# Kernel optimization log

Measured on AMD Instinct MI355X. Metric: run time of the kernel, lower is better.

The kernel has to match this reference:

```python
import jax, jax.numpy as jnp
import numpy as np

NHEAD, DK, DV, DMODEL, L = 8, 64, 64, 512, 32

def setup_inputs() -> dict:
    key = jax.random.key(0)
    ks = jax.random.split(key, 9)
    B, N = 4, 2048
    s = 1.0 / np.sqrt(DMODEL)
    return {
        "q": jax.random.normal(ks[0], (B, N, DMODEL), jnp.float32),
        "k": jax.random.normal(ks[1], (B, N, DMODEL), jnp.float32),
        "v": jax.random.normal(ks[2], (B, N, DMODEL), jnp.float32),
        "Wq": jax.random.normal(ks[3], (DMODEL, NHEAD * DK), jnp.float32) * s,
        "Wk": jax.random.normal(ks[4], (DMODEL, NHEAD * DK), jnp.float32) * s,
        "Wv": jax.random.normal(ks[5], (DMODEL, NHEAD * DV), jnp.float32) * s,
        "Wfc": jax.random.normal(ks[6], (NHEAD * DV, DMODEL), jnp.float32) * s,
        "ln_g": jnp.ones((DMODEL,), jnp.float32),
        "ln_b": jnp.zeros((DMODEL,), jnp.float32),
    }

def reference(q, k, v, Wq, Wk, Wv, Wfc, ln_g, ln_b):
    B, Nq, _ = q.shape
    residual = q
    # project and split heads: [B, H, N, d]
    qh = (q @ Wq).reshape(B, Nq, NHEAD, DK).transpose(0, 2, 1, 3)
    kh = (k @ Wk).reshape(B, k.shape[1], NHEAD, DK).transpose(0, 2, 1, 3)
    vh = (v @ Wv).reshape(B, v.shape[1], NHEAD, DV).transpose(0, 2, 1, 3)
    # scaled dot-product scores and softmax over keys
    attn = jnp.einsum('bhqd,bhkd->bhqk', qh / jnp.sqrt(jnp.float32(DK)), kh)
    attn = jax.nn.softmax(attn, axis=-1)
    # AWG: keep entries >= l-th largest per row, renormalize
    threshold = jax.lax.top_k(attn, L)[0][..., -1:]  # [B,H,Nq,1]
    W = jnp.where(attn >= threshold, attn, 0.0)
    W_out = W / jnp.sum(W, axis=-1, keepdims=True)
    out = jnp.einsum('bhqk,bhkd->bhqd', W_out, vh)
    out = out.transpose(0, 2, 1, 3).reshape(B, Nq, NHEAD * DV)
    out = out @ Wfc + residual
    # LayerNorm, eps=1e-6
    mu = jnp.mean(out, axis=-1, keepdims=True)
    var = jnp.var(out, axis=-1, keepdims=True)
    return (out - mu) / jnp.sqrt(var + 1e-6) * ln_g + ln_b
```

## Files before the change

### kernel.cpp

```cpp
#include <hip/hip_runtime.h>
#include <hip/hip_fp16.h>

#define BATCH 4
#define NSEQ 2048
#define DMODEL 512
#define NHEAD 8
#define HDIM 64
#define LSEL 32
#define SROWU 2056
#define MAXL 128

typedef __attribute__((ext_vector_type(8))) _Float16 f16x8;
typedef __attribute__((ext_vector_type(4))) float f32x4;

__device__ inline ushort f2h(float x) { __half h = __float2half(x); return *reinterpret_cast<ushort*>(&h); }
__device__ inline uint h2sort(ushort h) { return (h & 0x8000u) ? (uint)(h ^ 0xFFFFu) : (uint)(h | 0x8000u); }
__device__ inline float sort2f(uint su) {
    ushort hb = (su & 0x8000u) ? (ushort)(su ^ 0x8000u) : (ushort)(su ^ 0xFFFFu);
    __half th; *reinterpret_cast<ushort*>(&th) = hb;
    return __half2float(th);
}

__global__ __launch_bounds__(256) void cvtW_kernel(
    const float* __restrict__ Wq, const float* __restrict__ Wk,
    const float* __restrict__ Wv, const float* __restrict__ Wfc,
    ushort* __restrict__ Wt)
{
    const int z = blockIdx.y;
    const float* W = (z == 0) ? Wq : (z == 1) ? Wk : (z == 2) ? Wv : Wfc;
    ushort* O = Wt + (size_t)z * DMODEL * DMODEL;
    const int gt = blockIdx.x * 256 + threadIdx.x;
    const int n = gt & 511;
    const int kc = (gt >> 9) * 16;
    uint pk[8];
#pragma unroll
    for (int i = 0; i < 8; ++i) {
        uint lo = f2h(W[(size_t)(kc + 2 * i) * DMODEL + n]);
        uint hi = f2h(W[(size_t)(kc + 2 * i + 1) * DMODEL + n]);
        pk[i] = lo | (hi << 16);
    }
    uint4 u0 = {pk[0], pk[1], pk[2], pk[3]};
    uint4 u1 = {pk[4], pk[5], pk[6], pk[7]};
    *(uint4*)(O + (size_t)n * DMODEL + kc) = u0;
    *(uint4*)(O + (size_t)n * DMODEL + kc + 8) = u1;
}

template<int MODE>
__global__ __launch_bounds__(256, 2) void hgemm_kernel(
    const float* __restrict__ Fq, const float* __restrict__ Fk, const float* __restrict__ Fv,
    const ushort* __restrict__ A16,
    const ushort* __restrict__ Wt,
    ushort* __restrict__ O0, ushort* __restrict__ O1, ushort* __restrict__ O2,
    float* __restrict__ Ofc)
{
    __shared__ ushort Ah[64][40];
    __shared__ ushort Bh[512][40];

    const int tid = threadIdx.x;
    const int wave = tid >> 6, lane = tid & 63;
    const int lr = lane & 15, lg = lane >> 4;
    const int bm = blockIdx.x * 64;
    const int z = blockIdx.y;

    const float* Af = (MODE == 0) ? (z == 0 ? Fq : z == 1 ? Fk : Fv) : nullptr;
    const ushort* Wz = Wt + (size_t)((MODE == 0) ? z : 3) * (DMODEL * DMODEL);

    f32x4 acc[4][8];
#pragma unroll
    for (int i = 0; i < 4; ++i)
#pragma unroll
        for (int j = 0; j < 8; ++j) acc[i][j] = (f32x4){0.f, 0.f, 0.f, 0.f};

    const int sar = tid >> 2, sak = (tid & 3) * 8;

    for (int k0 = 0; k0 < DMODEL; k0 += 32) {
        __syncthreads();
        if (MODE == 0) {
            float4 fa = *(const float4*)(Af + (size_t)(bm + sar) * DMODEL + k0 + sak);
            float4 fb = *(const float4*)(Af + (size_t)(bm + sar) * DMODEL + k0 + sak + 4);
            uint4 pk;
            pk.x = (uint)f2h(fa.x) | ((uint)f2h(fa.y) << 16);
            pk.y = (uint)f2h(fa.z) | ((uint)f2h(fa.w) << 16);
            pk.z = (uint)f2h(fb.x) | ((uint)f2h(fb.y) << 16);
            pk.w = (uint)f2h(fb.z) | ((uint)f2h(fb.w) << 16);
            *(uint4*)&Ah[sar][sak] = pk;
        } else {
            *(uint4*)&Ah[sar][sak] = *(const uint4*)(A16 + (size_t)(bm + sar) * DMODEL + k0 + sak);
        }
#pragma unroll
        for (int i = 0; i < 8; ++i) {
            int n = sar + 64 * i;
            *(uint4*)&Bh[n][sak] = *(const uint4*)(Wz + (size_t)n * DMODEL + k0 + sak);
        }
        __syncthreads();
        f16x8 af[4];
#pragma unroll
        for (int fr = 0; fr < 4; ++fr) af[fr] = *(const f16x8*)&Ah[fr * 16 + lr][lg * 8];
#pragma unroll
        for (int fc2 = 0; fc2 < 8; ++fc2) {
            f16x8 bf = *(const f16x8*)&Bh[wave * 128 + fc2 * 16 + lr][lg * 8];
#pragma unroll
            for (int fr = 0; fr < 4; ++fr)
                acc[fr][fc2] = __builtin_amdgcn_mfma_f32_16x16x32_f16(af[fr], bf, acc[fr][fc2], 0, 0, 0);
        }
    }

    if (MODE == 1) {
#pragma unroll
        for (int fr = 0; fr < 4; ++fr)
#pragma unroll
            for (int fc2 = 0; fc2 < 8; ++fc2)
#pragma unroll
                for (int r = 0; r < 4; ++r)
                    Ofc[(size_t)(bm + fr * 16 + lg * 4 + r) * DMODEL + wave * 128 + fc2 * 16 + lr] = acc[fr][fc2][r];
        return;
    }

    ushort* O = (z == 0) ? O0 : (z == 1) ? O1 : O2;
    const int b = bm >> 11;
    const int nseq0 = bm & (NSEQ - 1);
    ushort* smw = (ushort*)&Bh[0][0] + wave * (64 * 72);
#pragma unroll
    for (int hp = 0; hp < 2; ++hp) {
        __syncthreads();
#pragma unroll
        for (int f4 = 0; f4 < 4; ++f4) {
            int fc2 = hp * 4 + f4;
            int nl = f4 * 16 + lr;
#pragma unroll
            for (int fr = 0; fr < 4; ++fr)
#pragma unroll
                for (int r = 0; r < 4; ++r)
                    smw[(fr * 16 + lg * 4 + r) * 72 + nl] = f2h(acc[fr][fc2][r]);
        }
        __syncthreads();
        const int h = wave * 2 + hp;
        ushort* obase = O + ((size_t)(b * NHEAD + h) * NSEQ + nseq0) * HDIM;
#pragma unroll
        for (int i = 0; i < 8; ++i) {
            int m = i * 8 + (lane >> 3);
            int dc = (lane & 7) * 8;
            *(uint4*)(obase + (size_t)m * HDIM + dc) = *(const uint4*)(smw + m * 72 + dc);
        }
    }
}

__device__ inline int wave_sum6(int c) {
    int tot = (int)__popcll(__ballot(c & 1));
    tot += (int)__popcll(__ballot(c & 2)) << 1;
    tot += (int)__popcll(__ballot(c & 4)) << 2;
    tot += (int)__popcll(__ballot(c & 8)) << 3;
    tot += (int)__popcll(__ballot(c & 16)) << 4;
    tot += (int)__popcll(__ballot(c & 32)) << 5;
    return tot;
}

__device__ uint full_thr(const ushort* Sr, int lane, uint lo0) {
    uint flo = lo0, fhi = 0xFFFFu;
#pragma unroll 1
    for (int it2 = 0; it2 < 16; ++it2) {
        uint mid = (flo + fhi + 1) >> 1, M = mid << 16;
        int cl = 0;
#pragma unroll
        for (int it = 0; it < 4; ++it) {
            uint4 r4 = *(const uint4*)(Sr + it * 512 + lane * 8);
            cl += ((r4.x << 16) >= M) + ((r4.x & 0xFFFF0000u) >= M);
            cl += ((r4.y << 16) >= M) + ((r4.y & 0xFFFF0000u) >= M);
            cl += ((r4.z << 16) >= M) + ((r4.z & 0xFFFF0000u) >= M);
            cl += ((r4.w << 16) >= M) + ((r4.w & 0xFFFF0000u) >= M);
        }
        bool ge = wave_sum6(cl) >= LSEL;
        flo = ge ? mid : flo;
        fhi = ge ? fhi : mid - 1;
    }
    return flo;
}

__device__ int recount(const ushort* Sr, int lane, uint th) {
    int cs = 0;
#pragma unroll
    for (int it = 0; it < 4; ++it) {
        uint4 r4 = *(const uint4*)(Sr + it * 512 + lane * 8);
        cs += ((r4.x << 16) >= th) + ((r4.x & 0xFFFF0000u) >= th);
        cs += ((r4.y << 16) >= th) + ((r4.y & 0xFFFF0000u) >= th);
        cs += ((r4.z << 16) >= th) + ((r4.z & 0xFFFF0000u) >= th);
        cs += ((r4.w << 16) >= th) + ((r4.w & 0xFFFF0000u) >= th);
    }
    return cs;
}

__device__ float extract_big(const ushort* Sr, int lane, uint th, float Mv,
                             int pre, ushort* li, float* lwp)
{
    const float L2E = 1.4426950408889634f;
    float wp = 0.f;
    int pos = pre;
#pragma unroll
    for (int it = 0; it < 4; ++it) {
        uint4 r4 = *(const uint4*)(Sr + it * 512 + lane * 8);
        uint ib = (uint)(it * 512 + lane * 8);
        uint wds[4] = {r4.x, r4.y, r4.z, r4.w};
#pragma unroll
        for (int c = 0; c < 4; ++c) {
            uint vL = wds[c] << 16, vH = wds[c] & 0xFFFF0000u;
            if (vL >= th) {
                float w = exp2f((sort2f(vL >> 16) - Mv) * L2E);
                if (pos < MAXL) { li[pos] = (ushort)(ib + c * 2); lwp[pos] = w; wp += w; }
                ++pos;
            }
            if (vH >= th) {
                float w = exp2f((sort2f(vH >> 16) - Mv) * L2E);
                if (pos < MAXL) { li[pos] = (ushort)(ib + c * 2 + 1); lwp[pos] = w; wp += w; }
                ++pos;
            }
        }
    }
#pragma unroll
    for (int off = 32; off >= 1; off >>= 1) wp += __shfl_xor(wp, off);
    return wp;
}

__device__ float extract_fast(uint t0, uint t1, uint t2, uint t3,
                              uint th, float Mv, int pre, ushort* li, float* lwp)
{
    const float L2E = 1.4426950408889634f;
    float wp = 0.f;
    uint tt[4] = {t0, t1, t2, t3};
#pragma unroll
    for (int i = 0; i < 4; ++i) {
        if (tt[i] >= th) {
            int pos = pre + i;
            float w = exp2f((sort2f(tt[i] >> 16) - Mv) * L2E);
            if (pos < MAXL) { li[pos] = (ushort)(tt[i] & 0xFFFFu); lwp[pos] = w; wp += w; }
        }
    }
#pragma unroll
    for (int off = 32; off >= 1; off >>= 1) wp += __shfl_xor(wp, off);
    return wp;
}

#define INS5(T0, T1, T2, T3, T4, P) { \
    uint m1_ = min(P, T0); T0 = max(P, T0); \
    uint m2_ = min(m1_, T1); T1 = max(m1_, T1); \
    uint m3_ = min(m2_, T2); T2 = max(m2_, T2); \
    uint m4_ = min(m3_, T3); T3 = max(m3_, T3); \
    T4 = max(m4_, T4); }

__global__ __launch_bounds__(512, 4) void attn_kernel(
    const ushort* __restrict__ qh, const ushort* __restrict__ kh,
    const ushort* __restrict__ vh, ushort* __restrict__ ao)
{
    __shared__ __align__(16) ushort Sbuf[16 * SROWU];
    __shared__ ushort lidx[16][MAXL];
    __shared__ float  lw[16][MAXL];

    const int tid = threadIdx.x;
    const int wave = tid >> 6;
    const int lane = tid & 63;
    const int bh = blockIdx.y;
    const int q0 = blockIdx.x * 16;
    const int lr = lane & 15;
    const int lg = lane >> 4;

    const ushort* Qb = qh + ((size_t)bh * NSEQ + q0) * HDIM;
    const ushort* Kb = kh + (size_t)bh * NSEQ * HDIM;

    f16x8 qf0 = *(const f16x8*)(Qb + lr * HDIM + lg * 8);
    f16x8 qf1 = *(const f16x8*)(Qb + lr * HDIM + 32 + lg * 8);

    for (int t = 0; t < 16; ++t) {
        const int k0 = wave * 256 + t * 16;
        const ushort* Kt = Kb + (size_t)k0 * HDIM;
        f16x8 a0 = *(const f16x8*)(Kt + lr * HDIM + lg * 8);
        f16x8 a1 = *(const f16x8*)(Kt + lr * HDIM + 32 + lg * 8);
        f32x4 acc = {0.f, 0.f, 0.f, 0.f};
        acc = __builtin_amdgcn_mfma_f32_16x16x32_f16(a0, qf0, acc, 0, 0, 0);
        acc = __builtin_amdgcn_mfma_f32_16x16x32_f16(a1, qf1, acc, 0, 0, 0);
        uint2 pk;
        pk.x = h2sort(f2h(acc[0] * 0.125f)) | (h2sort(f2h(acc[1] * 0.125f)) << 16);
        pk.y = h2sort(f2h(acc[2] * 0.125f)) | (h2sort(f2h(acc[3] * 0.125f)) << 16);
        *(uint2*)&Sbuf[lr * SROWU + k0 + lg * 4] = pk;
    }
    __syncthreads();

    const ushort* Vb = vh + (size_t)bh * NSEQ * HDIM;
    const int b = bh >> 3, hh = bh & 7;
    const unsigned long long below = (1ULL << lane) - 1ULL;

    const int qrA = wave * 2, qrB = qrA + 1;
    const ushort* SrA = &Sbuf[qrA * SROWU];
    const ushort* SrB = &Sbuf[qrB * SROWU];

    uint a0 = 0, a1 = 0, a2 = 0, a3 = 0, a4 = 0;
    uint b0 = 0, b1 = 0, b2 = 0, b3 = 0, b4 = 0;
#pragma unroll
    for (int it = 0; it < 4; ++it) {
        uint4 ra = *(const uint4*)(SrA + it * 512 + lane * 8);
        uint4 rb = *(const uint4*)(SrB + it * 512 + lane * 8);
        uint ib = (uint)(it * 512 + lane * 8);
        uint p;
        p = (ra.x << 16) | (ib + 0); INS5(a0, a1, a2, a3, a4, p);
        p = (ra.x & 0xFFFF0000u) | (ib + 1); INS5(a0, a1, a2, a3, a4, p);
        p = (ra.y << 16) | (ib + 2); INS5(a0, a1, a2, a3, a4, p);
        p = (ra.y & 0xFFFF0000u) | (ib + 3); INS5(a0, a1, a2, a3, a4, p);
        p = (ra.z << 16) | (ib + 4); INS5(a0, a1, a2, a3, a4, p);
        p = (ra.z & 0xFFFF0000u) | (ib + 5); INS5(a0, a1, a2, a3, a4, p);
        p = (ra.w << 16) | (ib + 6); INS5(a0, a1, a2, a3, a4, p);
        p = (ra.w & 0xFFFF0000u) | (ib + 7); INS5(a0, a1, a2, a3, a4, p);
        p = (rb.x << 16) | (ib + 0); INS5(b0, b1, b2, b3, b4, p);
        p = (rb.x & 0xFFFF0000u) | (ib + 1); INS5(b0, b1, b2, b3, b4, p);
        p = (rb.y << 16) | (ib + 2); INS5(b0, b1, b2, b3, b4, p);
        p = (rb.y & 0xFFFF0000u) | (ib + 3); INS5(b0, b1, b2, b3, b4, p);
        p = (rb.z << 16) | (ib + 4); INS5(b0, b1, b2, b3, b4, p);
        p = (rb.z & 0xFFFF0000u) | (ib + 5); INS5(b0, b1, b2, b3, b4, p);
        p = (rb.w << 16) | (ib + 6); INS5(b0, b1, b2, b3, b4, p);
        p = (rb.w & 0xFFFF0000u) | (ib + 7); INS5(b0, b1, b2, b3, b4, p);
    }

    uint mxA = a0, mxB = b0;
#pragma unroll
    for (int off = 32; off >= 1; off >>= 1) {
        mxA = max(mxA, (uint)__shfl_xor((int)mxA, off));
        mxB = max(mxB, (uint)__shfl_xor((int)mxB, off));
    }
    const float MvA = sort2f(mxA >> 16), MvB = sort2f(mxB >> 16);

    uint loA = 0, hiA = 0xFFFFu, loB = 0, hiB = 0xFFFFu;
#pragma unroll
    for (int it = 0; it < 16; ++it) {
        uint midA = (loA + hiA + 1) >> 1, MA = midA << 16;
        uint midB = (loB + hiB + 1) >> 1, MB = midB << 16;
        int cA = (a0 >= MA) + (a1 >= MA) + (a2 >= MA) + (a3 >= MA);
        int cB = (b0 >= MB) + (b1 >= MB) + (b2 >= MB) + (b3 >= MB);
        int totA = (int)__popcll(__ballot(cA & 1)) + ((int)__popcll(__ballot(cA & 2)) << 1)
                 + ((int)__popcll(__ballot(cA & 4)) << 2);
        int totB = (int)__popcll(__ballot(cB & 1)) + ((int)__popcll(__ballot(cB & 2)) << 1)
                 + ((int)__popcll(__ballot(cB & 4)) << 2);
        bool geA = totA >= LSEL, geB = totB >= LSEL;
        loA = geA ? midA : loA; hiA = geA ? hiA : midA - 1;
        loB = geB ? midB : loB; hiB = geB ? hiB : midB - 1;
    }

    uint thA = loA << 16, thB = loB << 16;

    const bool missA = __any(a4 >= thA);
    const bool missB = __any(b4 >= thB);

    int cselA, cselB;
    if (!missA) {
        cselA = (a0 >= thA) + (a1 >= thA) + (a2 >= thA) + (a3 >= thA);
    } else {
        int cgt = recount(SrA, lane, thA + 0x10000u);
        if (wave_sum6(cgt) >= LSEL) { loA = full_thr(SrA, lane, loA); thA = loA << 16; }
        cselA = recount(SrA, lane, thA);
    }
    if (!missB) {
        cselB = (b0 >= thB) + (b1 >= thB) + (b2 >= thB) + (b3 >= thB);
    } else {
        int cgt = recount(SrB, lane, thB + 0x10000u);
        if (wave_sum6(cgt) >= LSEL) { loB = full_thr(SrB, lane, loB); thB = loB << 16; }
        cselB = recount(SrB, lane, thB);
    }

    int preA = 0, totA2 = 0, preB = 0, totB2 = 0;
#pragma unroll
    for (int bb = 0; bb < 6; ++bb) {
        unsigned long long mA = __ballot((cselA >> bb) & 1);
        unsigned long long mB = __ballot((cselB >> bb) & 1);
        preA += (int)__popcll(mA & below) << bb; totA2 += (int)__popcll(mA) << bb;
        preB += (int)__popcll(mB & below) << bb; totB2 += (int)__popcll(mB) << bb;
    }

    const float wsumA = missA
        ? extract_big(SrA, lane, thA, MvA, preA, &lidx[qrA][0], &lw[qrA][0])
        : extract_fast(a0, a1, a2, a3, thA, MvA, preA, &lidx[qrA][0], &lw[qrA][0]);
    const float wsumB = missB
        ? extract_big(SrB, lane, thB, MvB, preB, &lidx[qrB][0], &lw[qrB][0])
        : extract_fast(b0, b1, b2, b3, thB, MvB, preB, &lidx[qrB][0], &lw[qrB][0]);

    const int nkA = (totA2 < MAXL) ? totA2 : MAXL;
    const int nkB = (totB2 < MAXL) ? totB2 : MAXL;

    const int half = lane >> 5;
    const int dp = lane & 31;
    const int qrMy = qrA + half;
    const int nkMy = half ? nkB : nkA;
    const float wsMy = half ? wsumB : wsumA;
    const __half2* V2 = reinterpret_cast<const __half2*>(Vb);

    float ox = 0.f, oy = 0.f;
    int j = 0;
    for (; j + 4 <= nkMy; j += 4) {
        int i0 = lidx[qrMy][j + 0]; float w0 = lw[qrMy][j + 0];
        int i1 = lidx[qrMy][j + 1]; float w1 = lw[qrMy][j + 1];
        int i2 = lidx[qrMy][j + 2]; float w2 = lw[qrMy][j + 2];
        int i3 = lidx[qrMy][j + 3]; float w3 = lw[qrMy][j + 3];
        float2 v0 = __half22float2(V2[(size_t)i0 * 32 + dp]);
        float2 v1 = __half22float2(V2[(size_t)i1 * 32 + dp]);
        float2 v2 = __half22float2(V2[(size_t)i2 * 32 + dp]);
        float2 v3 = __half22float2(V2[(size_t)i3 * 32 + dp]);
        ox += w0 * v0.x + w1 * v1.x + w2 * v2.x + w3 * v3.x;
        oy += w0 * v0.y + w1 * v1.y + w2 * v2.y + w3 * v3.y;
    }
    for (; j < nkMy; ++j) {
        int i0 = lidx[qrMy][j]; float w0 = lw[qrMy][j];
        float2 v0 = __half22float2(V2[(size_t)i0 * 32 + dp]);
        ox += w0 * v0.x; oy += w0 * v0.y;
    }

    const float inv = 1.f / wsMy;
    uint opk = (uint)f2h(ox * inv) | ((uint)f2h(oy * inv) << 16);
    *(uint*)(ao + ((size_t)(b * NSEQ) + q0 + qrMy) * DMODEL + hh * HDIM + dp * 2) = opk;
}

__global__ __launch_bounds__(256) void ln_kernel(
    const float* __restrict__ fcr, const float* __restrict__ resid,
    const float* __restrict__ g, const float* __restrict__ bta, float* __restrict__ out)
{
    const int row = blockIdx.x * 4 + (threadIdx.x >> 6);
    const int lane = threadIdx.x & 63;
    const size_t base = (size_t)row * DMODEL + lane * 8;
    float4 xa = *(const float4*)(fcr + base);
    float4 xb = *(const float4*)(fcr + base + 4);
    float4 ra = *(const float4*)(resid + base);
    float4 rb = *(const float4*)(resid + base + 4);
    xa.x += ra.x; xa.y += ra.y; xa.z += ra.z; xa.w += ra.w;
    xb.x += rb.x; xb.y += rb.y; xb.z += rb.z; xb.w += rb.w;
    float sum = xa.x + xa.y + xa.z + xa.w + xb.x + xb.y + xb.z + xb.w;
    float sq = xa.x * xa.x + xa.y * xa.y + xa.z * xa.z + xa.w * xa.w
             + xb.x * xb.x + xb.y * xb.y + xb.z * xb.z + xb.w * xb.w;
#pragma unroll
    for (int off = 32; off >= 1; off >>= 1) {
        sum += __shfl_xor(sum, off);
        sq += __shfl_xor(sq, off);
    }
    float mean = sum * (1.f / 512.f);
    float var = sq * (1.f / 512.f) - mean * mean;
    float rstd = rsqrtf(var + 1e-6f);
    float4 ga = *(const float4*)(g + lane * 8);
    float4 gb = *(const float4*)(g + lane * 8 + 4);
    float4 ba = *(const float4*)(bta + lane * 8);
    float4 bb = *(const float4*)(bta + lane * 8 + 4);
    float4 oa, ob;
    oa.x = (xa.x - mean) * rstd * ga.x + ba.x;
    oa.y = (xa.y - mean) * rstd * ga.y + ba.y;
    oa.z = (xa.z - mean) * rstd * ga.z + ba.z;
    oa.w = (xa.w - mean) * rstd * ga.w + ba.w;
    ob.x = (xb.x - mean) * rstd * gb.x + bb.x;
    ob.y = (xb.y - mean) * rstd * gb.y + bb.y;
    ob.z = (xb.z - mean) * rstd * gb.z + bb.z;
    ob.w = (xb.w - mean) * rstd * gb.w + bb.w;
    *(float4*)(out + base) = oa;
    *(float4*)(out + base + 4) = ob;
}

extern "C" void kernel_launch(void* const* d_in, const int* in_sizes, int n_in,
                              void* d_out, int out_size, void* d_ws, size_t ws_size,
                              hipStream_t stream)
{
    (void)in_sizes; (void)n_in; (void)out_size; (void)ws_size;

    const float* q   = (const float*)d_in[0];
    const float* k   = (const float*)d_in[1];
    const float* v   = (const float*)d_in[2];
    const float* Wq  = (const float*)d_in[3];
    const float* Wk  = (const float*)d_in[4];
    const float* Wv  = (const float*)d_in[5];
    const float* Wfc = (const float*)d_in[6];
    const float* g   = (const float*)d_in[7];
    const float* b   = (const float*)d_in[8];
    float* out = (float*)d_out;

    const size_t SZ = (size_t)BATCH * NSEQ * DMODEL;
    const size_t WSZ = (size_t)DMODEL * DMODEL;
    ushort* Wt = (ushort*)d_ws;
    ushort* qh = Wt + 4 * WSZ;
    ushort* kh = qh + SZ;
    ushort* vh = kh + SZ;
    ushort* ao = vh + SZ;
    float* fc_raw = (float*)qh;

    cvtW_kernel<<<dim3(64, 4), 256, 0, stream>>>(Wq, Wk, Wv, Wfc, Wt);
    hgemm_kernel<0><<<dim3(128, 3), 256, 0, stream>>>(q, k, v, nullptr, Wt, qh, kh, vh, nullptr);
    attn_kernel<<<dim3(NSEQ / 16, BATCH * NHEAD), 512, 0, stream>>>(qh, kh, vh, ao);
    hgemm_kernel<1><<<dim3(128, 1), 256, 0, stream>>>(nullptr, nullptr, nullptr, ao, Wt, nullptr, nullptr, nullptr, fc_raw);
    ln_kernel<<<(BATCH * NSEQ) / 4, 256, 0, stream>>>(fc_raw, q, g, b, out);
}
```

Baseline: 333.0 us.

## Process one query row per wave with 8-row attention blocks

Halves the query rows per attention block to 8, so each wave runs top-k selection and weighted V gather for a single row instead of two. Raises the occupancy hint to 8 blocks per CU and splits the V gather across the two half-waves with a shuffle reduction. This is meant to shorten the serial per-wave selection chain and reduce register/LDS pressure. The cost is that the 16-wide MFMA computes duplicated query rows, and the K reads and QK work double across the larger grid.

```diff
diff --git a/kernel.cpp b/kernel.cpp
--- a/kernel.cpp
+++ b/kernel.cpp
@@ -9,6 +9,7 @@
 #define LSEL 32
 #define SROWU 2056
 #define MAXL 128
+#define QROWS 8
 
 typedef __attribute__((ext_vector_type(8))) _Float16 f16x8;
 typedef __attribute__((ext_vector_type(4))) float f32x4;
@@ -246,27 +247,27 @@
     uint m4_ = min(m3_, T3); T3 = max(m3_, T3); \
     T4 = max(m4_, T4); }
 
-__global__ __launch_bounds__(512, 4) void attn_kernel(
+__global__ __launch_bounds__(512, 8) void attn_kernel(
     const ushort* __restrict__ qh, const ushort* __restrict__ kh,
     const ushort* __restrict__ vh, ushort* __restrict__ ao)
 {
-    __shared__ __align__(16) ushort Sbuf[16 * SROWU];
-    __shared__ ushort lidx[16][MAXL];
-    __shared__ float  lw[16][MAXL];
+    __shared__ __align__(16) ushort Sbuf[QROWS * SROWU];
+    __shared__ ushort lidx[QROWS][MAXL];
+    __shared__ float  lw[QROWS][MAXL];
 
     const int tid = threadIdx.x;
     const int wave = tid >> 6;
     const int lane = tid & 63;
     const int bh = blockIdx.y;
-    const int q0 = blockIdx.x * 16;
+    const int q0 = blockIdx.x * QROWS;
     const int lr = lane & 15;
     const int lg = lane >> 4;
 
     const ushort* Qb = qh + ((size_t)bh * NSEQ + q0) * HDIM;
     const ushort* Kb = kh + (size_t)bh * NSEQ * HDIM;
 
-    f16x8 qf0 = *(const f16x8*)(Qb + lr * HDIM + lg * 8);
-    f16x8 qf1 = *(const f16x8*)(Qb + lr * HDIM + 32 + lg * 8);
+    f16x8 qf0 = *(const f16x8*)(Qb + (lr & 7) * HDIM + lg * 8);
+    f16x8 qf1 = *(const f16x8*)(Qb + (lr & 7) * HDIM + 32 + lg * 8);
 
     for (int t = 0; t < 16; ++t) {
         const int k0 = wave * 256 + t * 16;
@@ -276,10 +277,12 @@
         f32x4 acc = {0.f, 0.f, 0.f, 0.f};
         acc = __builtin_amdgcn_mfma_f32_16x16x32_f16(a0, qf0, acc, 0, 0, 0);
         acc = __builtin_amdgcn_mfma_f32_16x16x32_f16(a1, qf1, acc, 0, 0, 0);
-        uint2 pk;
-        pk.x = h2sort(f2h(acc[0] * 0.125f)) | (h2sort(f2h(acc[1] * 0.125f)) << 16);
-        pk.y = h2sort(f2h(acc[2] * 0.125f)) | (h2sort(f2h(acc[3] * 0.125f)) << 16);
-        *(uint2*)&Sbuf[lr * SROWU + k0 + lg * 4] = pk;
+        if (lr < QROWS) {
+            uint2 pk;
+            pk.x = h2sort(f2h(acc[0] * 0.125f)) | (h2sort(f2h(acc[1] * 0.125f)) << 16);
+            pk.y = h2sort(f2h(acc[2] * 0.125f)) | (h2sort(f2h(acc[3] * 0.125f)) << 16);
+            *(uint2*)&Sbuf[lr * SROWU + k0 + lg * 4] = pk;
+        }
     }
     __syncthreads();
 
@@ -287,16 +290,13 @@
     const int b = bh >> 3, hh = bh & 7;
     const unsigned long long below = (1ULL << lane) - 1ULL;
 
-    const int qrA = wave * 2, qrB = qrA + 1;
-    const ushort* SrA = &Sbuf[qrA * SROWU];
-    const ushort* SrB = &Sbuf[qrB * SROWU];
+    const int qr = wave;
+    const ushort* Sr = &Sbuf[qr * SROWU];
 
     uint a0 = 0, a1 = 0, a2 = 0, a3 = 0, a4 = 0;
-    uint b0 = 0, b1 = 0, b2 = 0, b3 = 0, b4 = 0;
 #pragma unroll
     for (int it = 0; it < 4; ++it) {
-        uint4 ra = *(const uint4*)(SrA + it * 512 + lane * 8);
-        uint4 rb = *(const uint4*)(SrB + it * 512 + lane * 8);
+        uint4 ra = *(const uint4*)(Sr + it * 512 + lane * 8);
         uint ib = (uint)(it * 512 + lane * 8);
         uint p;
         p = (ra.x << 16) | (ib + 0); INS5(a0, a1, a2, a3, a4, p);
@@ -307,94 +307,64 @@
         p = (ra.z & 0xFFFF0000u) | (ib + 5); INS5(a0, a1, a2, a3, a4, p);
         p = (ra.w << 16) | (ib + 6); INS5(a0, a1, a2, a3, a4, p);
         p = (ra.w & 0xFFFF0000u) | (ib + 7); INS5(a0, a1, a2, a3, a4, p);
-        p = (rb.x << 16) | (ib + 0); INS5(b0, b1, b2, b3, b4, p);
-        p = (rb.x & 0xFFFF0000u) | (ib + 1); INS5(b0, b1, b2, b3, b4, p);
-        p = (rb.y << 16) | (ib + 2); INS5(b0, b1, b2, b3, b4, p);
-        p = (rb.y & 0xFFFF0000u) | (ib + 3); INS5(b0, b1, b2, b3, b4, p);
-        p = (rb.z << 16) | (ib + 4); INS5(b0, b1, b2, b3, b4, p);
-        p = (rb.z & 0xFFFF0000u) | (ib + 5); INS5(b0, b1, b2, b3, b4, p);
-        p = (rb.w << 16) | (ib + 6); INS5(b0, b1, b2, b3, b4, p);
-        p = (rb.w & 0xFFFF0000u) | (ib + 7); INS5(b0, b1, b2, b3, b4, p);
-    }
-
-    uint mxA = a0, mxB = b0;
-#pragma unroll
-    for (int off = 32; off >= 1; off >>= 1) {
-        mxA = max(mxA, (uint)__shfl_xor((int)mxA, off));
-        mxB = max(mxB, (uint)__shfl_xor((int)mxB, off));
-    }
-    const float MvA = sort2f(mxA >> 16), MvB = sort2f(mxB >> 16);
-
-    uint loA = 0, hiA = 0xFFFFu, loB = 0, hiB = 0xFFFFu;
+    }
+
+    uint mx = a0;
+#pragma unroll
+    for (int off = 32; off >= 1; off >>= 1) mx = max(mx, (uint)__shfl_xor((int)mx, off));
+    const float Mv = sort2f(mx >> 16);
+
+    uint lo = 0, hi = 0xFFFFu;
 #pragma unroll
     for (int it = 0; it < 16; ++it) {
-        uint midA = (loA + hiA + 1) >> 1, MA = midA << 16;
-        uint midB = (loB + hiB + 1) >> 1, MB = midB << 16;
-        int cA = (a0 >= MA) + (a1 >= MA) + (a2 >= MA) + (a3 >= MA);
-        int cB = (b0 >= MB) + (b1 >= MB) + (b2 >= MB) + (b3 >= MB);
-        int totA = (int)__popcll(__ballot(cA & 1)) + ((int)__popcll(__ballot(cA & 2)) << 1)
-                 + ((int)__popcll(__ballot(cA & 4)) << 2);
-        int totB = (int)__popcll(__ballot(cB & 1)) + ((int)__popcll(__ballot(cB & 2)) << 1)
-                 + ((int)__popcll(__ballot(cB & 4)) << 2);
-        bool geA = totA >= LSEL, geB = totB >= LSEL;
-        loA = geA ? midA : loA; hiA = geA ? hiA : midA - 1;
-        loB = geB ? midB : loB; hiB = geB ? hiB : midB - 1;
-    }
-
-    uint thA = loA << 16, thB = loB << 16;
-
-    const bool missA = __any(a4 >= thA);
-    const bool missB = __any(b4 >= thB);
-
-    int cselA, cselB;
-    if (!missA) {
-        cselA = (a0 >= thA) + (a1 >= thA) + (a2 >= thA) + (a3 >= thA);
+        uint mid = (lo + hi + 1) >> 1, M = mid << 16;
+        int c = (a0 >= M) + (a1 >= M) + (a2 >= M) + (a3 >= M);
+        int tot = (int)__popcll(__ballot(c & 1)) + ((int)__popcll(__ballot(c & 2)) << 1)
+                + ((int)__popcll(__ballot(c & 4)) << 2);
+        bool ge = tot >= LSEL;
+        lo = ge ? mid : lo;
+        hi = ge ? hi : mid - 1;
+    }
+    uint th = lo << 16;
+
+    const bool miss = __any(a4 >= th);
+
+    int csel;
+    if (!miss) {
+        csel = (a0 >= th) + (a1 >= th) + (a2 >= th) + (a3 >= th);
     } else {
-        int cgt = recount(SrA, lane, thA + 0x10000u);
-        if (wave_sum6(cgt) >= LSEL) { loA = full_thr(SrA, lane, loA); thA = loA << 16; }
-        cselA = recount(SrA, lane, thA);
-    }
-    if (!missB) {
-        cselB = (b0 >= thB) + (b1 >= thB) + (b2 >= thB) + (b3 >= thB);
-    } else {
-        int cgt = recount(SrB, lane, thB + 0x10000u);
-        if (wave_sum6(cgt) >= LSEL) { loB = full_thr(SrB, lane, loB); thB = loB << 16; }
-        cselB = recount(SrB, lane, thB);
-    }
-
-    int preA = 0, totA2 = 0, preB = 0, totB2 = 0;
+        int cgt = recount(Sr, lane, th + 0x10000u);
+        if (wave_sum6(cgt) >= LSEL) { lo = full_thr(Sr, lane, lo); th = lo << 16; }
+        csel = recount(Sr, lane, th);
+    }
+
+    int pre = 0, totsel = 0;
 #pragma unroll
     for (int bb = 0; bb < 6; ++bb) {
-        unsigned long long mA = __ballot((cselA >> bb) & 1);
-        unsigned long long mB = __ballot((cselB >> bb) & 1);
-        preA += (int)__popcll(mA & below) << bb; totA2 += (int)__popcll(mA) << bb;
-        preB += (int)__popcll(mB & below) << bb; totB2 += (int)__popcll(mB) << bb;
-    }
-
-    const float wsumA = missA
-        ? extract_big(SrA, lane, thA, MvA, preA, &lidx[qrA][0], &lw[qrA][0])
-        : extract_fast(a0, a1, a2, a3, thA, MvA, preA, &lidx[qrA][0], &lw[qrA][0]);
-    const float wsumB = missB
-        ? extract_big(SrB, lane, thB, MvB, preB, &lidx[qrB][0], &lw[qrB][0])
-        : extract_fast(b0, b1, b2, b3, thB, MvB, preB, &lidx[qrB][0], &lw[qrB][0]);
-
-    const int nkA = (totA2 < MAXL) ? totA2 : MAXL;
-    const int nkB = (totB2 < MAXL) ? totB2 : MAXL;
+        unsigned long long m = __ballot((csel >> bb) & 1);
+        pre += (int)__popcll(m & below) << bb;
+        totsel += (int)__popcll(m) << bb;
+    }
+
+    const float wsum = miss
+        ? extract_big(Sr, lane, th, Mv, pre, &lidx[qr][0], &lw[qr][0])
+        : extract_fast(a0, a1, a2, a3, th, Mv, pre, &lidx[qr][0], &lw[qr][0]);
+
+    const int nk = (totsel < MAXL) ? totsel : MAXL;
+
+    asm volatile("s_waitcnt lgkmcnt(0)" ::: "memory");
 
     const int half = lane >> 5;
     const int dp = lane & 31;
-    const int qrMy = qrA + half;
-    const int nkMy = half ? nkB : nkA;
-    const float wsMy = half ? wsumB : wsumA;
     const __half2* V2 = reinterpret_cast<const __half2*>(Vb);
 
     float ox = 0.f, oy = 0.f;
-    int j = 0;
-    for (; j + 4 <= nkMy; j += 4) {
-        int i0 = lidx[qrMy][j + 0]; float w0 = lw[qrMy][j + 0];
-        int i1 = lidx[qrMy][j + 1]; float w1 = lw[qrMy][j + 1];
-        int i2 = lidx[qrMy][j + 2]; float w2 = lw[qrMy][j + 2];
-        int i3 = lidx[qrMy][j + 3]; float w3 = lw[qrMy][j + 3];
+    int j = half;
+    for (; j + 6 < nk; j += 8) {
+        int i0 = lidx[qr][j + 0]; float w0 = lw[qr][j + 0];
+        int i1 = lidx[qr][j + 2]; float w1 = lw[qr][j + 2];
+        int i2 = lidx[qr][j + 4]; float w2 = lw[qr][j + 4];
+        int i3 = lidx[qr][j + 6]; float w3 = lw[qr][j + 6];
         float2 v0 = __half22float2(V2[(size_t)i0 * 32 + dp]);
         float2 v1 = __half22float2(V2[(size_t)i1 * 32 + dp]);
         float2 v2 = __half22float2(V2[(size_t)i2 * 32 + dp]);
@@ -402,15 +372,19 @@
         ox += w0 * v0.x + w1 * v1.x + w2 * v2.x + w3 * v3.x;
         oy += w0 * v0.y + w1 * v1.y + w2 * v2.y + w3 * v3.y;
     }
-    for (; j < nkMy; ++j) {
-        int i0 = lidx[qrMy][j]; float w0 = lw[qrMy][j];
+    for (; j < nk; j += 2) {
+        int i0 = lidx[qr][j]; float w0 = lw[qr][j];
         float2 v0 = __half22float2(V2[(size_t)i0 * 32 + dp]);
         ox += w0 * v0.x; oy += w0 * v0.y;
     }
-
-    const float inv = 1.f / wsMy;
-    uint opk = (uint)f2h(ox * inv) | ((uint)f2h(oy * inv) << 16);
-    *(uint*)(ao + ((size_t)(b * NSEQ) + q0 + qrMy) * DMODEL + hh * HDIM + dp * 2) = opk;
+    ox += __shfl_xor(ox, 32);
+    oy += __shfl_xor(oy, 32);
+
+    if (half == 0) {
+        const float inv = 1.f / wsum;
+        uint opk = (uint)f2h(ox * inv) | ((uint)f2h(oy * inv) << 16);
+        *(uint*)(ao + ((size_t)(b * NSEQ) + q0 + qr) * DMODEL + hh * HDIM + dp * 2) = opk;
+    }
 }
 
 __global__ __launch_bounds__(256) void ln_kernel(
@@ -482,7 +456,7 @@
 
     cvtW_kernel<<<dim3(64, 4), 256, 0, stream>>>(Wq, Wk, Wv, Wfc, Wt);
     hgemm_kernel<0><<<dim3(128, 3), 256, 0, stream>>>(q, k, v, nullptr, Wt, qh, kh, vh, nullptr);
-    attn_kernel<<<dim3(NSEQ / 16, BATCH * NHEAD), 512, 0, stream>>>(qh, kh, vh, ao);
+    attn_kernel<<<dim3(NSEQ / QROWS, BATCH * NHEAD), 512, 0, stream>>>(qh, kh, vh, ao);
     hgemm_kernel<1><<<dim3(128, 1), 256, 0, stream>>>(nullptr, nullptr, nullptr, ao, Wt, nullptr, nullptr, nullptr, fc_raw);
     ln_kernel<<<(BATCH * NSEQ) / 4, 256, 0, stream>>>(fc_raw, q, g, b, out);
 }
```

New measurement: 390.1 us. 1.17x slower.
